# Kernel optimization log

Measured on AMD Instinct MI355X. Metric: run time of the kernel, lower is better.

The kernel has to match this reference:

```python
import jax, jax.numpy as jnp
import numpy as np

N = 8388608          # number of samples (2**23)
T_MAX = 100000       # number of distinct time values -> ~84 ties per time


def setup_inputs() -> dict:
    key = jax.random.key(0)
    k1, k2, k3 = jax.random.split(key, 3)
    inp = jax.random.normal(k1, (N,), dtype=jnp.float32)            # log hazards
    target = jax.random.randint(k2, (N,), 0, T_MAX, dtype=jnp.int32)  # times
    weight = jax.random.randint(k3, (N,), 0, 2, dtype=jnp.int32)      # event indicator
    return {"input": inp, "target": target, "weight": weight}


def _cox_efron_npll(log_hz, time, event):
    """Negative Cox partial log-likelihood with Efron tie correction, mean reduction.

    Faithful to torchsurv's _partial_likelihood_efron: per unique time j,
    pll_j = sum_{i in H_j} log_hz_i - sum_{l=0}^{m_j-1} log(D_j - (l/m_j)*T_j)
    where H_j = events at time j, D_j = sum of exp(log_hz) over risk set (t>=t_j),
    T_j = sum of exp(log_hz) over H_j, m_j = |H_j|; loss = -mean over j with m_j>0.
    """
    n = log_hz.shape[0]
    order = jnp.argsort(time)                       # sort by time (group-sum math is tie-order invariant)
    t = time[order]
    lh = log_hz[order]
    ev = event[order].astype(lh.dtype)

    # group id per sample: 0..(num_unique-1), padded groups beyond that are empty
    new_grp = jnp.concatenate([jnp.zeros((1,), jnp.int32), (t[1:] != t[:-1]).astype(jnp.int32)])
    seg = jnp.cumsum(new_grp)                       # [n] int32

    hz = jnp.exp(lh)
    grp_hz = jax.ops.segment_sum(hz, seg, num_segments=n)          # sum exp per time group
    denom_naive = jnp.cumsum(grp_hz[::-1])[::-1]                   # risk-set sums (suffix over groups)
    m = jax.ops.segment_sum(ev, seg, num_segments=n)               # events per group
    log_nom = jax.ops.segment_sum(lh * ev, seg, num_segments=n)    # sum of log_hz over H_j
    ties = jax.ops.segment_sum(hz * ev, seg, num_segments=n)       # sum of exp over H_j

    # rank l in [0, m_j) of each event within its group
    csum_e = jnp.cumsum(ev)
    events_before = jnp.concatenate([jnp.zeros((1,), lh.dtype), jnp.cumsum(m)[:-1]])
    rank = csum_e - 1.0 - events_before[seg]
    mg = jnp.maximum(m[seg], 1.0)
    term = jnp.where(ev > 0.0,
                     jnp.log(denom_naive[seg] - (rank / mg) * ties[seg]),
                     0.0)
    log_denom = jax.ops.segment_sum(term, seg, num_segments=n)

    include = (m > 0.0).astype(lh.dtype)
    pll = jnp.where(m > 0.0, log_nom - log_denom, 0.0)
    # reduction='mean': -pll.nanmean() over groups that contain events
    return -(jnp.sum(pll) / jnp.sum(include))


def reference(input, target, weight):
    return _cox_efron_npll(input, target, weight)
```

## Files before the change

kernel.cpp:

```cpp
#include <hip/hip_runtime.h>

#define TMAXV 100000
#define CHUNK 256
#define NCHUNK ((TMAXV + CHUNK - 1) / CHUNK)
#define WB 256
#define LOGWB 8
#define SB ((TMAXV + WB - 1) / WB)
#define TILE 4096
#define RPT 16
#define KS 4
#define CAP 4096

__device__ __forceinline__ float block_reduce_sum(float v, float* sdata) {
    int lane = threadIdx.x & 63;
    int wid  = threadIdx.x >> 6;
    #pragma unroll
    for (int off = 32; off > 0; off >>= 1)
        v += __shfl_down(v, off, 64);
    if (lane == 0) sdata[wid] = v;
    __syncthreads();
    if (wid == 0) {
        v = (lane < 4) ? sdata[lane] : 0.0f;
        v += __shfl_down(v, 2, 64);
        v += __shfl_down(v, 1, 64);
    }
    return v;
}


__global__ void count_kernel(const int* __restrict__ tgt,
                             int* __restrict__ blkcnt, int n, int nt) {
    __shared__ int lc[SB];
    for (int i = threadIdx.x; i < SB; i += blockDim.x) lc[i] = 0;
    __syncthreads();
    int tile = blockIdx.x;
    int lo = tile * TILE;
    int hi = min(n, lo + TILE);
    for (int i = lo + threadIdx.x; i < hi; i += blockDim.x)
        atomicAdd(&lc[tgt[i] >> LOGWB], 1);
    __syncthreads();
    for (int s = threadIdx.x; s < SB; s += blockDim.x)
        blkcnt[s * nt + tile] = lc[s];
}

__global__ void tile_scan_kernel(const int* __restrict__ blkcnt,
                                 int* __restrict__ tilebase,
                                 int* __restrict__ totals, int nt) {
    __shared__ int ls[256];
    int s   = blockIdx.x;
    int tid = threadIdx.x;
    int run = 0;
    for (int t0 = 0; t0 < nt; t0 += 256) {
        int t = t0 + tid;
        int c = (t < nt) ? blkcnt[s * nt + t] : 0;
        ls[tid] = c;
        __syncthreads();
        for (int off = 1; off < 256; off <<= 1) {
            int a = (tid >= off) ? ls[tid - off] : 0;
            __syncthreads();
            ls[tid] += a;
            __syncthreads();
        }
        int incl = ls[tid];
        int tot  = ls[255];
        if (t < nt) tilebase[s * nt + t] = run + incl - c;
        run += tot;
        __syncthreads();
    }
    if (tid == 0) totals[s] = run;
}

__global__ void bucket_base_kernel(const int* __restrict__ totals,
                                   int* __restrict__ base, int n) {
    __shared__ int ls[512];
    int tid = threadIdx.x;
    int c = (tid < SB) ? totals[tid] : 0;
    ls[tid] = c;
    __syncthreads();
    for (int off = 1; off < 512; off <<= 1) {
        int a = (tid >= off) ? ls[tid - off] : 0;
        __syncthreads();
        ls[tid] += a;
        __syncthreads();
    }
    if (tid < SB) base[tid] = ls[tid] - c;
    if (tid == 0) base[SB] = n;
}

__global__ void scatter_kernel(const float* __restrict__ lh,
                               const int*   __restrict__ tgt,
                               const int*   __restrict__ ev,
                               const int*   __restrict__ tilebase,
                               const int*   __restrict__ base,
                               uint2* __restrict__ sorted, int n, int nt) {
    __shared__ uint2 recs[TILE];
    __shared__ int lcnt[SB];
    __shared__ int pfx[SB];
    __shared__ int lrank[SB];
    __shared__ int tb[SB];
    __shared__ int ls[512];
    int tid  = threadIdx.x;
    int tile = blockIdx.x;
    int lo   = tile * TILE;
    int cnt_here = min(TILE, n - lo);

    for (int s = tid; s < SB; s += 256) {
        lcnt[s]  = 0;
        lrank[s] = 0;
        tb[s]    = base[s] + tilebase[s * nt + tile];
    }
    __syncthreads();

    unsigned ry[RPT];
    unsigned rx[RPT];
    #pragma unroll
    for (int k = 0; k < RPT; ++k) {
        int i = lo + k * 256 + tid;
        if (i < n) {
            int t = tgt[i];
            ry[k] = ((unsigned)t << 1) | (unsigned)(ev[i] & 1);
            rx[k] = __float_as_uint(lh[i]);
            atomicAdd(&lcnt[t >> LOGWB], 1);
        } else {
            ry[k] = 0xFFFFFFFFu;
        }
    }
    __syncthreads();

    int c0   = (tid < SB) ? lcnt[tid] : 0;
    int idx1 = tid + 256;
    int c1   = (idx1 < SB) ? lcnt[idx1] : 0;
    ls[tid]  = c0;
    ls[idx1] = c1;
    __syncthreads();
    for (int off = 1; off < 512; off <<= 1) {
        int a0 = (tid  >= off) ? ls[tid  - off] : 0;
        int a1 = (idx1 >= off) ? ls[idx1 - off] : 0;
        __syncthreads();
        ls[tid]  += a0;
        ls[idx1] += a1;
        __syncthreads();
    }
    if (tid  < SB) pfx[tid]  = ls[tid]  - c0;
    if (idx1 < SB) pfx[idx1] = ls[idx1] - c1;
    __syncthreads();

    #pragma unroll
    for (int k = 0; k < RPT; ++k) {
        if (ry[k] != 0xFFFFFFFFu) {
            int b = (int)(ry[k] >> (LOGWB + 1));
            int r = atomicAdd(&lrank[b], 1);
            recs[pfx[b] + r] = make_uint2(rx[k], ry[k]);
        }
    }
    __syncthreads();

    for (int p = tid; p < cnt_here; p += 256) {
        uint2 rec = recs[p];
        int b = (int)(rec.y >> (LOGWB + 1));
        sorted[tb[b] + (p - pfx[b])] = rec;
    }
}

__global__ void bucket_hist_kernel(const uint2* __restrict__ sorted,
                                   const int*   __restrict__ base,
                                   float* __restrict__ partials,
                                   double* __restrict__ acc) {
    __shared__ uint2 recs[CAP];
    __shared__ unsigned cnt[WB];
    __shared__ unsigned rankc[WB];
    __shared__ unsigned pfx[WB];
    __shared__ unsigned ls[WB];
    __shared__ float sdata[4];
    int tid = threadIdx.x;
    int b   = blockIdx.x >> 2;
    int k   = blockIdx.x & (KS - 1);
    int lo0 = base[b], len = base[b + 1] - lo0;
    int lo  = lo0 + (int)(((long long)len * k) / KS);
    int hi  = lo0 + (int)(((long long)len * (k + 1)) / KS);

    float sh = 0.f, cm = 0.f, th = 0.f, lx = 0.f;

    for (int c0 = lo; c0 < hi; c0 += CAP) {
        int c1 = min(hi, c0 + CAP);
        cnt[tid] = 0; rankc[tid] = 0;
        __syncthreads();

        unsigned sy[16], sx[16];
        #pragma unroll
        for (int u = 0; u < 16; ++u) {
            int i = c0 + u * 256 + tid;
            if (i < c1) {
                uint2 rec = sorted[i];
                sx[u] = rec.x; sy[u] = rec.y;
                atomicAdd(&cnt[(rec.y >> 1) & (WB - 1)], 1u);
            } else {
                sy[u] = 0xFFFFFFFFu;
            }
        }
        __syncthreads();

        unsigned c = cnt[tid];
        ls[tid] = c;
        __syncthreads();
        for (int off = 1; off < 256; off <<= 1) {
            unsigned a = (tid >= off) ? ls[tid - off] : 0u;
            __syncthreads();
            ls[tid] += a;
            __syncthreads();
        }
        pfx[tid] = ls[tid] - c;
        __syncthreads();

        #pragma unroll
        for (int u = 0; u < 16; ++u) {
            if (sy[u] != 0xFFFFFFFFu) {
                int slot = (int)((sy[u] >> 1) & (WB - 1));
                unsigned r = atomicAdd(&rankc[slot], 1u);
                recs[pfx[slot] + r] = make_uint2(sx[u], sy[u]);
            }
        }
        __syncthreads();

        int s0 = (int)pfx[tid], e0 = s0 + (int)cnt[tid];
        for (int p = s0; p < e0; ++p) {
            uint2 rec = recs[p];
            float x = __uint_as_float(rec.x);
            float h = __expf(x);
            sh += h;
            if (rec.y & 1u) { cm += 1.0f; th += h; lx += x; }
        }
        __syncthreads();
    }

    float* pbase = partials + (size_t)blockIdx.x * 3 * WB;
    pbase[0 * WB + tid] = sh;
    pbase[1 * WB + tid] = cm;
    pbase[2 * WB + tid] = th;

    float rl = block_reduce_sum(lx, sdata);
    if (tid == 0) atomicAdd(&acc[2], (double)rl);
}

__global__ void merge_kernel(const float* __restrict__ partials,
                             float* __restrict__ sum_hz,
                             float* __restrict__ mcnt,
                             float* __restrict__ ties,
                             float* __restrict__ chunk_sum) {
    __shared__ float sdata[4];
    int tid = threadIdx.x;
    int b   = blockIdx.x;
    float sh = 0.f, cm = 0.f, th = 0.f;
    #pragma unroll
    for (int k = 0; k < KS; ++k) {
        const float* pbase = partials + (size_t)(b * KS + k) * 3 * WB;
        sh += pbase[0 * WB + tid];
        cm += pbase[1 * WB + tid];
        th += pbase[2 * WB + tid];
    }
    int t = (b << LOGWB) + tid;
    float shv = (t < TMAXV) ? sh : 0.f;
    if (t < TMAXV) {
        sum_hz[t] = sh;
        mcnt[t]   = cm;
        ties[t]   = th;
    }
    float cs = block_reduce_sum(shv, sdata);
    if (tid == 0) chunk_sum[b] = cs;
}

__global__ void chunk_scan_kernel(const float* __restrict__ chunk_sum,
                                  double* __restrict__ chunk_off) {
    __shared__ double ds[512];
    int tid = threadIdx.x;
    double own = (tid < NCHUNK) ? (double)chunk_sum[tid] : 0.0;
    ds[tid] = own;
    __syncthreads();
    for (int off = 1; off < 512; off <<= 1) {
        double add = (tid + off < 512) ? ds[tid + off] : 0.0;
        __syncthreads();
        ds[tid] += add;
        __syncthreads();
    }
    if (tid < NCHUNK) chunk_off[tid] = ds[tid] - own;
}

__global__ void pll_suffix_kernel(const float* __restrict__ sum_hz,
                                  const float* __restrict__ mcnt,
                                  const float* __restrict__ ties,
                                  const double* __restrict__ chunk_off,
                                  double* __restrict__ acc) {
    __shared__ float sf[CHUNK];
    __shared__ float sdata[4];
    __shared__ float sdata2[4];
    int tid = threadIdx.x;
    int t   = blockIdx.x * CHUNK + tid;
    float v = (t < TMAXV) ? sum_hz[t] : 0.0f;
    sf[tid] = v;
    __syncthreads();
    for (int off = 1; off < CHUNK; off <<= 1) {
        float add = (tid + off < CHUNK) ? sf[tid + off] : 0.0f;
        __syncthreads();
        sf[tid] += add;
        __syncthreads();
    }
    float pll = 0.0f, inc = 0.0f;
    if (t < TMAXV) {
        float mv = mcnt[t];
        if (mv > 0.5f) {
            float D    = (float)(chunk_off[blockIdx.x] + (double)sf[tid]);
            float T    = ties[t];
            int   mi   = (int)(mv + 0.5f);
            float step = T / mv;
            float s = 0.0f;
            for (int l = 0; l < mi; ++l)
                s += __logf(D - (float)l * step);
            pll = -s;
            inc = 1.0f;
        }
    }
    float rp = block_reduce_sum(pll, sdata);
    __syncthreads();
    float ri = block_reduce_sum(inc, sdata2);
    if (threadIdx.x == 0) {
        atomicAdd(&acc[0], (double)rp);
        atomicAdd(&acc[1], (double)ri);
    }
}

__global__ void finalize_kernel(const double* __restrict__ acc,
                                float* __restrict__ out) {
    double cnt = acc[1];
    out[0] = (cnt > 0.0) ? (float)(-(acc[0] + acc[2]) / cnt) : 0.0f;
}

__global__ void hist_kernel(const float* __restrict__ lh,
                            const int*   __restrict__ tgt,
                            const int*   __restrict__ ev,
                            float* __restrict__ sum_hz,
                            float* __restrict__ mcnt,
                            float* __restrict__ log_nom,
                            float* __restrict__ ties,
                            int n) {
    int i = blockIdx.x * blockDim.x + threadIdx.x;
    if (i >= n) return;
    float x = lh[i];
    int   t = tgt[i];
    int   e = ev[i];
    float h = __expf(x);
    unsafeAtomicAdd(&sum_hz[t], h);
    if (e) {
        unsafeAtomicAdd(&mcnt[t], 1.0f);
        unsafeAtomicAdd(&log_nom[t], x);
        unsafeAtomicAdd(&ties[t], h);
    }
}

__global__ void chunk_sum_kernel(const float* __restrict__ sum_hz,
                                 float* __restrict__ chunk_sum) {
    __shared__ float sdata[4];
    int i = blockIdx.x * CHUNK + threadIdx.x;
    float v = (i < TMAXV) ? sum_hz[i] : 0.0f;
    v = block_reduce_sum(v, sdata);
    if (threadIdx.x == 0) chunk_sum[blockIdx.x] = v;
}

__global__ void pll_kernel(const float* __restrict__ mcnt,
                           const float* __restrict__ log_nom,
                           const float* __restrict__ ties,
                           const float* __restrict__ sum_hz,
                           const double* __restrict__ chunk_off,
                           double* __restrict__ acc) {
    __shared__ float sf[CHUNK];
    __shared__ float sdata[4];
    __shared__ float sdata2[4];
    int tid = threadIdx.x;
    int t   = blockIdx.x * CHUNK + tid;
    float v = (t < TMAXV) ? sum_hz[t] : 0.0f;
    sf[tid] = v;
    __syncthreads();
    for (int off = 1; off < CHUNK; off <<= 1) {
        float add = (tid + off < CHUNK) ? sf[tid + off] : 0.0f;
        __syncthreads();
        sf[tid] += add;
        __syncthreads();
    }
    float pll = 0.0f, inc = 0.0f;
    if (t < TMAXV) {
        float mv = mcnt[t];
        if (mv > 0.5f) {
            float D    = (float)(chunk_off[blockIdx.x] + (double)sf[tid]);
            float T    = ties[t];
            int   mi   = (int)(mv + 0.5f);
            float step = T / mv;
            float s = 0.0f;
            for (int l = 0; l < mi; ++l)
                s += __logf(D - (float)l * step);
            pll = log_nom[t] - s;
            inc = 1.0f;
        }
    }
    float rp = block_reduce_sum(pll, sdata);
    __syncthreads();
    float ri = block_reduce_sum(inc, sdata2);
    if (threadIdx.x == 0) {
        atomicAdd(&acc[0], (double)rp);
        atomicAdd(&acc[1], (double)ri);
    }
}

extern "C" void kernel_launch(void* const* d_in, const int* in_sizes, int n_in,
                              void* d_out, int out_size, void* d_ws, size_t ws_size,
                              hipStream_t stream) {
    const float* lh  = (const float*)d_in[0];
    const int*   tgt = (const int*)d_in[1];
    const int*   ev  = (const int*)d_in[2];
    float*       out = (float*)d_out;
    int n  = in_sizes[0];
    int nt = (n + TILE - 1) / TILE;

    char* ws = (char*)d_ws;
    size_t off = 0;
    auto take = [&](size_t bytes, size_t align) {
        off = (off + align - 1) & ~(align - 1);
        size_t r = off; off += bytes; return r;
    };
    size_t o_acc    = take(32, 16);
    size_t o_sum    = take((size_t)TMAXV * 4, 16);
    size_t o_m      = take((size_t)TMAXV * 4, 16);
    size_t o_ties   = take((size_t)TMAXV * 4, 16);
    size_t o_base   = take((size_t)(SB + 1) * 4, 4);
    size_t o_totals = take((size_t)SB * 4, 4);
    size_t o_csum   = take((size_t)NCHUNK * 4, 16);
    size_t o_coff   = take((size_t)NCHUNK * 8, 8);
    size_t o_blkcnt = take((size_t)nt * SB * 4, 16);
    size_t o_tbase  = take((size_t)nt * SB * 4, 16);
    size_t o_sorted = take((size_t)n * 8, 16);
    size_t part_sz  = (size_t)SB * KS * 3 * WB * 4;
    size_t o_part   = o_blkcnt;
    size_t need     = off;
    if (o_part + part_sz > need) need = o_part + part_sz;

    if (ws_size >= need) {
        double* acc      = (double*)(ws + o_acc);
        float*  sum_hz   = (float*)(ws + o_sum);
        float*  mcnt     = (float*)(ws + o_m);
        float*  ties     = (float*)(ws + o_ties);
        int*    base     = (int*)(ws + o_base);
        int*    totals   = (int*)(ws + o_totals);
        float*  chunk_sum= (float*)(ws + o_csum);
        double* chunk_off= (double*)(ws + o_coff);
        int*    blkcnt   = (int*)(ws + o_blkcnt);
        int*    tilebase = (int*)(ws + o_tbase);
        uint2*  sorted   = (uint2*)(ws + o_sorted);
        float*  partials = (float*)(ws + o_part);

        hipMemsetAsync(d_ws, 0, 32, stream);

        count_kernel<<<nt, 256, 0, stream>>>(tgt, blkcnt, n, nt);
        tile_scan_kernel<<<SB, 256, 0, stream>>>(blkcnt, tilebase, totals, nt);
        bucket_base_kernel<<<1, 512, 0, stream>>>(totals, base, n);
        scatter_kernel<<<nt, 256, 0, stream>>>(lh, tgt, ev, tilebase, base, sorted, n, nt);
        bucket_hist_kernel<<<SB * KS, 256, 0, stream>>>(sorted, base, partials, acc);
        merge_kernel<<<SB, 256, 0, stream>>>(partials, sum_hz, mcnt, ties, chunk_sum);
        chunk_scan_kernel<<<1, 512, 0, stream>>>(chunk_sum, chunk_off);
        pll_suffix_kernel<<<NCHUNK, 256, 0, stream>>>(sum_hz, mcnt, ties, chunk_off, acc);
        finalize_kernel<<<1, 1, 0, stream>>>(acc, out);
    } else {
        size_t f = 0;
        auto ftake = [&](size_t bytes, size_t align) {
            f = (f + align - 1) & ~(align - 1);
            size_t r = f; f += bytes; return r;
        };
        size_t f_acc  = ftake(32, 16);
        size_t f_sum  = ftake((size_t)TMAXV * 4, 16);
        size_t f_m    = ftake((size_t)TMAXV * 4, 16);
        size_t f_ln   = ftake((size_t)TMAXV * 4, 16);
        size_t f_ties = ftake((size_t)TMAXV * 4, 16);
        size_t zb     = f;
        size_t f_csum = ftake((size_t)NCHUNK * 4, 16);
        size_t f_coff = ftake((size_t)NCHUNK * 8, 8);

        double* acc     = (double*)(ws + f_acc);
        float*  sum_hz  = (float*)(ws + f_sum);
        float*  mcnt    = (float*)(ws + f_m);
        float*  log_nom = (float*)(ws + f_ln);
        float*  ties    = (float*)(ws + f_ties);
        float*  chunk_sum = (float*)(ws + f_csum);
        double* chunk_off = (double*)(ws + f_coff);

        hipMemsetAsync(d_ws, 0, zb, stream);

        hist_kernel<<<(n + 255) / 256, 256, 0, stream>>>(lh, tgt, ev, sum_hz, mcnt, log_nom, ties, n);
        chunk_sum_kernel<<<NCHUNK, 256, 0, stream>>>(sum_hz, chunk_sum);
        chunk_scan_kernel<<<1, 512, 0, stream>>>(chunk_sum, chunk_off);
        pll_kernel<<<NCHUNK, 256, 0, stream>>>(mcnt, log_nom, ties, sum_hz, chunk_off, acc);
        finalize_kernel<<<1, 1, 0, stream>>>(acc, out);
    }
}
```

Before: 265.1 us.

## Compact scattered records to signed exp value plus byte slot, histogram with LDS atomics

The scatter kernel now computes exp(log_hz) up front, encodes the event flag in the sign bit, and writes a 4-byte float plus a 1-byte within-bucket slot instead of an 8-byte record. The sum of event log-hazards also moves into the scatter kernel. The bucket histogram kernel drops its local counting sort and accumulates directly with shared-memory float atomics. This cuts intermediate global traffic from 8 to 5 bytes per sample and removes a sort pass, at the cost of LDS atomic contention, a per-element binary search in the scatter write-out, and byte-sized scattered stores.

```diff
diff --git a/kernel.cpp b/kernel.cpp
--- a/kernel.cpp
+++ b/kernel.cpp
@@ -9,7 +9,6 @@
 #define TILE 4096
 #define RPT 16
 #define KS 4
-#define CAP 4096
 
 __device__ __forceinline__ float block_reduce_sum(float v, float* sdata) {
     int lane = threadIdx.x & 63;
@@ -92,13 +91,17 @@
                                const int*   __restrict__ ev,
                                const int*   __restrict__ tilebase,
                                const int*   __restrict__ base,
-                               uint2* __restrict__ sorted, int n, int nt) {
-    __shared__ uint2 recs[TILE];
+                               float* __restrict__ val,
+                               unsigned char* __restrict__ slotArr,
+                               double* __restrict__ acc, int n, int nt) {
+    __shared__ float fv[TILE];
+    __shared__ unsigned char fs[TILE];
     __shared__ int lcnt[SB];
     __shared__ int pfx[SB];
     __shared__ int lrank[SB];
     __shared__ int tb[SB];
     __shared__ int ls[512];
+    __shared__ float sdata[4];
     int tid  = threadIdx.x;
     int tile = blockIdx.x;
     int lo   = tile * TILE;
@@ -111,18 +114,23 @@
     }
     __syncthreads();
 
-    unsigned ry[RPT];
-    unsigned rx[RPT];
+    float    rv[RPT];
+    unsigned rt[RPT];
+    float xl = 0.f;
     #pragma unroll
     for (int k = 0; k < RPT; ++k) {
         int i = lo + k * 256 + tid;
         if (i < n) {
             int t = tgt[i];
-            ry[k] = ((unsigned)t << 1) | (unsigned)(ev[i] & 1);
-            rx[k] = __float_as_uint(lh[i]);
+            int e = ev[i] & 1;
+            float x = lh[i];
+            float h = __expf(x);
+            rv[k] = e ? -h : h;
+            rt[k] = (unsigned)t;
+            if (e) xl += x;
             atomicAdd(&lcnt[t >> LOGWB], 1);
         } else {
-            ry[k] = 0xFFFFFFFFu;
+            rt[k] = 0xFFFFFFFFu;
         }
     }
     __syncthreads();
@@ -147,99 +155,60 @@
 
     #pragma unroll
     for (int k = 0; k < RPT; ++k) {
-        if (ry[k] != 0xFFFFFFFFu) {
-            int b = (int)(ry[k] >> (LOGWB + 1));
+        if (rt[k] != 0xFFFFFFFFu) {
+            int b = (int)(rt[k] >> LOGWB);
             int r = atomicAdd(&lrank[b], 1);
-            recs[pfx[b] + r] = make_uint2(rx[k], ry[k]);
+            int pos = pfx[b] + r;
+            fv[pos] = rv[k];
+            fs[pos] = (unsigned char)(rt[k] & (WB - 1));
         }
     }
     __syncthreads();
 
     for (int p = tid; p < cnt_here; p += 256) {
-        uint2 rec = recs[p];
-        int b = (int)(rec.y >> (LOGWB + 1));
-        sorted[tb[b] + (p - pfx[b])] = rec;
-    }
-}
-
-__global__ void bucket_hist_kernel(const uint2* __restrict__ sorted,
-                                   const int*   __restrict__ base,
-                                   float* __restrict__ partials,
-                                   double* __restrict__ acc) {
-    __shared__ uint2 recs[CAP];
-    __shared__ unsigned cnt[WB];
-    __shared__ unsigned rankc[WB];
-    __shared__ unsigned pfx[WB];
-    __shared__ unsigned ls[WB];
-    __shared__ float sdata[4];
-    int tid = threadIdx.x;
-    int b   = blockIdx.x >> 2;
-    int k   = blockIdx.x & (KS - 1);
+        int loB = 0, hiB = SB;
+        #pragma unroll
+        for (int it = 0; it < 9; ++it) {
+            int mid = (loB + hiB) >> 1;
+            if (pfx[mid] <= p) loB = mid; else hiB = mid;
+        }
+        int dst = tb[loB] + (p - pfx[loB]);
+        val[dst]     = fv[p];
+        slotArr[dst] = fs[p];
+    }
+
+    float rl = block_reduce_sum(xl, sdata);
+    if (tid == 0) atomicAdd(&acc[2], (double)rl);
+}
+
+__global__ void bucket_hist_kernel(const float* __restrict__ val,
+                                   const unsigned char* __restrict__ slotArr,
+                                   const int* __restrict__ base,
+                                   float* __restrict__ partials) {
+    __shared__ float hs[WB], hm[WB], ht[WB];
+    int tid = threadIdx.x;
+    hs[tid] = 0.f; hm[tid] = 0.f; ht[tid] = 0.f;
+    __syncthreads();
+    int b = blockIdx.x >> 2;
+    int k = blockIdx.x & (KS - 1);
     int lo0 = base[b], len = base[b + 1] - lo0;
     int lo  = lo0 + (int)(((long long)len * k) / KS);
     int hi  = lo0 + (int)(((long long)len * (k + 1)) / KS);
-
-    float sh = 0.f, cm = 0.f, th = 0.f, lx = 0.f;
-
-    for (int c0 = lo; c0 < hi; c0 += CAP) {
-        int c1 = min(hi, c0 + CAP);
-        cnt[tid] = 0; rankc[tid] = 0;
-        __syncthreads();
-
-        unsigned sy[16], sx[16];
-        #pragma unroll
-        for (int u = 0; u < 16; ++u) {
-            int i = c0 + u * 256 + tid;
-            if (i < c1) {
-                uint2 rec = sorted[i];
-                sx[u] = rec.x; sy[u] = rec.y;
-                atomicAdd(&cnt[(rec.y >> 1) & (WB - 1)], 1u);
-            } else {
-                sy[u] = 0xFFFFFFFFu;
-            }
-        }
-        __syncthreads();
-
-        unsigned c = cnt[tid];
-        ls[tid] = c;
-        __syncthreads();
-        for (int off = 1; off < 256; off <<= 1) {
-            unsigned a = (tid >= off) ? ls[tid - off] : 0u;
-            __syncthreads();
-            ls[tid] += a;
-            __syncthreads();
-        }
-        pfx[tid] = ls[tid] - c;
-        __syncthreads();
-
-        #pragma unroll
-        for (int u = 0; u < 16; ++u) {
-            if (sy[u] != 0xFFFFFFFFu) {
-                int slot = (int)((sy[u] >> 1) & (WB - 1));
-                unsigned r = atomicAdd(&rankc[slot], 1u);
-                recs[pfx[slot] + r] = make_uint2(sx[u], sy[u]);
-            }
-        }
-        __syncthreads();
-
-        int s0 = (int)pfx[tid], e0 = s0 + (int)cnt[tid];
-        for (int p = s0; p < e0; ++p) {
-            uint2 rec = recs[p];
-            float x = __uint_as_float(rec.x);
-            float h = __expf(x);
-            sh += h;
-            if (rec.y & 1u) { cm += 1.0f; th += h; lx += x; }
-        }
-        __syncthreads();
-    }
-
+    for (int i = lo + tid; i < hi; i += 256) {
+        float v = val[i];
+        int   s = (int)slotArr[i];
+        float h = fabsf(v);
+        unsafeAtomicAdd(&hs[s], h);
+        if (__float_as_uint(v) >> 31) {
+            unsafeAtomicAdd(&hm[s], 1.0f);
+            unsafeAtomicAdd(&ht[s], h);
+        }
+    }
+    __syncthreads();
     float* pbase = partials + (size_t)blockIdx.x * 3 * WB;
-    pbase[0 * WB + tid] = sh;
-    pbase[1 * WB + tid] = cm;
-    pbase[2 * WB + tid] = th;
-
-    float rl = block_reduce_sum(lx, sdata);
-    if (tid == 0) atomicAdd(&acc[2], (double)rl);
+    pbase[0 * WB + tid] = hs[tid];
+    pbase[1 * WB + tid] = hm[tid];
+    pbase[2 * WB + tid] = ht[tid];
 }
 
 __global__ void merge_kernel(const float* __restrict__ partials,
@@ -435,7 +404,8 @@
     size_t o_coff   = take((size_t)NCHUNK * 8, 8);
     size_t o_blkcnt = take((size_t)nt * SB * 4, 16);
     size_t o_tbase  = take((size_t)nt * SB * 4, 16);
-    size_t o_sorted = take((size_t)n * 8, 16);
+    size_t o_val    = take((size_t)n * 4, 16);
+    size_t o_slot   = take((size_t)n, 16);
     size_t part_sz  = (size_t)SB * KS * 3 * WB * 4;
     size_t o_part   = o_blkcnt;
     size_t need     = off;
@@ -452,7 +422,8 @@
         double* chunk_off= (double*)(ws + o_coff);
         int*    blkcnt   = (int*)(ws + o_blkcnt);
         int*    tilebase = (int*)(ws + o_tbase);
-        uint2*  sorted   = (uint2*)(ws + o_sorted);
+        float*  val      = (float*)(ws + o_val);
+        unsigned char* slotArr = (unsigned char*)(ws + o_slot);
         float*  partials = (float*)(ws + o_part);
 
         hipMemsetAsync(d_ws, 0, 32, stream);
@@ -460,8 +431,8 @@
         count_kernel<<<nt, 256, 0, stream>>>(tgt, blkcnt, n, nt);
         tile_scan_kernel<<<SB, 256, 0, stream>>>(blkcnt, tilebase, totals, nt);
         bucket_base_kernel<<<1, 512, 0, stream>>>(totals, base, n);
-        scatter_kernel<<<nt, 256, 0, stream>>>(lh, tgt, ev, tilebase, base, sorted, n, nt);
-        bucket_hist_kernel<<<SB * KS, 256, 0, stream>>>(sorted, base, partials, acc);
+        scatter_kernel<<<nt, 256, 0, stream>>>(lh, tgt, ev, tilebase, base, val, slotArr, acc, n, nt);
+        bucket_hist_kernel<<<SB * KS, 256, 0, stream>>>(val, slotArr, base, partials);
         merge_kernel<<<SB, 256, 0, stream>>>(partials, sum_hz, mcnt, ties, chunk_sum);
         chunk_scan_kernel<<<1, 512, 0, stream>>>(chunk_sum, chunk_off);
         pll_suffix_kernel<<<NCHUNK, 256, 0, stream>>>(sum_hz, mcnt, ties, chunk_off, acc);
```

After: 322.2 us. +21.5%, slower.
